# Kernel optimization log

Hardware: AMD Instinct MI355X
Metric: run time of the kernel (lower is better)

## Reference

```python
import jax, jax.numpy as jnp
import numpy as np

H = 1024          # hidden_size
D = 4             # num_domains
B, S = 8, 2048


def setup_inputs() -> dict:
    key = jax.random.key(0)
    ks = jax.random.split(key, 12)
    inp = {
        "sequence_embeddings": jax.random.normal(ks[0], (B, S, H), jnp.float32),
        "volatility": jax.random.uniform(ks[1], (B, S, 1), jnp.float32) * 0.02 + 0.005,
        "risk_factors": jax.random.normal(ks[2], (B, S, 1), jnp.float32) * 0.01,
        # learned parameters (match torch init scales)
        "domain_feature_weights": jax.random.normal(ks[3], (H, 2 * H), jnp.float32) * 0.02,
        "domain_feature_bias": jnp.zeros((2 * H,), jnp.float32),
        "domain_classifier_weights": jax.random.normal(ks[4], (2 * H, D), jnp.float32) * 0.02,
        "domain_classifier_bias": jnp.zeros((D,), jnp.float32),
        "volatility_router_weights": jax.random.normal(ks[5], (1, 8, D), jnp.float32) * 0.1,
        "volatility_router_bias": jnp.zeros((8, D), jnp.float32),
        "risk_router_weights": jax.random.normal(ks[6], (1, 8, D), jnp.float32) * 0.1,
        "risk_router_bias": jnp.zeros((8, D), jnp.float32),
        "stats_router_weights": jax.random.normal(ks[7], (3, 12, D), jnp.float32) * 0.1,
        "stats_router_bias": jnp.zeros((12, D), jnp.float32),
        "expert_weights": jax.random.normal(ks[8], (D, 2 * H, H), jnp.float32) * 0.02,
        "expert_bias": jnp.zeros((D, H), jnp.float32),
    }
    return inp


def reference(sequence_embeddings, volatility, risk_factors,
              domain_feature_weights, domain_feature_bias,
              domain_classifier_weights, domain_classifier_bias,
              volatility_router_weights, volatility_router_bias,
              risk_router_weights, risk_router_bias,
              stats_router_weights, stats_router_bias,
              expert_weights, expert_bias):
    x = sequence_embeddings
    # shared domain feature extractor: [B,S,H] -> [B,S,2H]
    feat = jnp.tanh(jnp.einsum('bsh,hf->bsf', x, domain_feature_weights) + domain_feature_bias)
    # content-based domain logits [B,S,D]
    dom_logits = jnp.einsum('bsf,fd->bsd', feat, domain_classifier_weights) + domain_classifier_bias
    # volatility router: scalar -> 8 hidden units per domain, tanh, sum -> [B,S,D]
    vol_logits = jnp.tanh(volatility[..., None] * volatility_router_weights[0]
                          + volatility_router_bias).sum(axis=-2)
    # risk router, same structure
    risk_logits = jnp.tanh(risk_factors[..., None] * risk_router_weights[0]
                           + risk_router_bias).sum(axis=-2)
    # per-token statistics (mean/std/max over feature dim) -> [B,S,3]
    stats = jnp.stack([x.mean(axis=-1), x.std(axis=-1), x.max(axis=-1)], axis=-1)
    stats_logits = jnp.tanh(jnp.einsum('bsc,ckd->bskd', stats, stats_router_weights)
                            + stats_router_bias).sum(axis=-2)
    # combined routing distribution over domains
    routing_probs = jax.nn.softmax(dom_logits + vol_logits + risk_logits + stats_logits, axis=-1)
    # dispatch every token through all D experts: [B,S,D,H]
    expert_out = jnp.einsum('bsf,dfh->bsdh', feat, expert_weights) + expert_bias
    # gated combine: [B,S,H]
    out = jnp.einsum('bsd,bsdh->bsh', routing_probs, expert_out)
    return out
```

## Files before the change

### kernel.cpp

```cpp
#include <hip/hip_runtime.h>
#include <hip/hip_bf16.h>
#include <cstdint>
#include <cstddef>

typedef __bf16 bf16_t;
typedef bf16_t bf16x8 __attribute__((ext_vector_type(8)));
typedef bf16_t bf16x4 __attribute__((ext_vector_type(4)));
typedef float  f32x4  __attribute__((ext_vector_type(4)));

#define TOK 16384
#define Hh  1024
#define F2  2048
#define NC  4096

__device__ __forceinline__ void gload_lds16(const bf16_t* g, bf16_t* lds) {
  __builtin_amdgcn_global_load_lds(
      (const __attribute__((address_space(1))) void*)g,
      (__attribute__((address_space(3))) void*)lds, 16, 0, 0);
}

__global__ __launch_bounds__(256)
void k_tr_wf(const float* __restrict__ in, bf16_t* __restrict__ out) {
  __shared__ float T[64][65];
  const int f0 = blockIdx.x * 64, h0 = blockIdx.y * 64;
  const int tid = threadIdx.x;
  const int c4 = (tid & 15) * 4, r = tid >> 4;
  #pragma unroll
  for (int p = 0; p < 4; ++p) {
    int hh = p * 16 + r;
    float4 v = *(const float4*)&in[(size_t)(h0 + hh) * F2 + f0 + c4];
    T[c4 + 0][hh] = v.x; T[c4 + 1][hh] = v.y; T[c4 + 2][hh] = v.z; T[c4 + 3][hh] = v.w;
  }
  __syncthreads();
  #pragma unroll
  for (int p = 0; p < 4; ++p) {
    int ff = p * 16 + r;
    bf16x4 o = { (bf16_t)T[ff][c4 + 0], (bf16_t)T[ff][c4 + 1],
                 (bf16_t)T[ff][c4 + 2], (bf16_t)T[ff][c4 + 3] };
    *(bf16x4*)&out[(size_t)(f0 + ff) * Hh + h0 + c4] = o;
  }
}

__global__ __launch_bounds__(256)
void k_tr_we(const float* __restrict__ in, bf16_t* __restrict__ out) {
  __shared__ float T[64][65];
  const int f0 = blockIdx.x * 64, h0 = blockIdx.y * 64, d = blockIdx.z;
  const float* ind = in + (size_t)d * F2 * Hh;
  const int tid = threadIdx.x;
  const int c4 = (tid & 15) * 4, r = tid >> 4;
  #pragma unroll
  for (int p = 0; p < 4; ++p) {
    int ff = p * 16 + r;
    float4 v = *(const float4*)&ind[(size_t)(f0 + ff) * Hh + h0 + c4];
    T[c4 + 0][ff] = v.x; T[c4 + 1][ff] = v.y; T[c4 + 2][ff] = v.z; T[c4 + 3][ff] = v.w;
  }
  __syncthreads();
  #pragma unroll
  for (int p = 0; p < 4; ++p) {
    int hh = p * 16 + r;
    bf16x4 o = { (bf16_t)T[hh][c4 + 0], (bf16_t)T[hh][c4 + 1],
                 (bf16_t)T[hh][c4 + 2], (bf16_t)T[hh][c4 + 3] };
    *(bf16x4*)&out[(size_t)((h0 + hh) * 4 + d) * F2 + f0 + c4] = o;
  }
}

__global__ void k_router_w(const float* __restrict__ x, const float* __restrict__ vol,
                           const float* __restrict__ risk, const float* __restrict__ clsb,
                           const float* __restrict__ vw, const float* __restrict__ vb,
                           const float* __restrict__ rw, const float* __restrict__ rb,
                           const float* __restrict__ sw, const float* __restrict__ sb,
                           bf16_t* __restrict__ xbf, float* __restrict__ LP,
                           int m0, int Tc) {
  int w = threadIdx.x >> 6, l = threadIdx.x & 63;
  int t = blockIdx.x * 4 + w;
  if (t >= Tc) return;
  int s = m0 + t;
  const float4* xr = (const float4*)(x + (size_t)s * Hh);
  bf16x4* xo = (bf16x4*)(xbf + (size_t)s * Hh);
  float sum = 0.f, sq = 0.f, mx = -1e30f;
  #pragma unroll
  for (int it = 0; it < 4; ++it) {
    float4 v = xr[it * 64 + l];
    sum += v.x + v.y + v.z + v.w;
    sq  += v.x * v.x + v.y * v.y + v.z * v.z + v.w * v.w;
    mx = fmaxf(mx, fmaxf(fmaxf(v.x, v.y), fmaxf(v.z, v.w)));
    bf16x4 o = { (bf16_t)v.x, (bf16_t)v.y, (bf16_t)v.z, (bf16_t)v.w };
    xo[it * 64 + l] = o;
  }
  #pragma unroll
  for (int off = 32; off; off >>= 1) {
    sum += __shfl_xor(sum, off, 64);
    sq  += __shfl_xor(sq,  off, 64);
    mx   = fmaxf(mx, __shfl_xor(mx, off, 64));
  }
  if (l < 4) {
    int d = l;
    float mean = sum * (1.0f / Hh);
    float var  = sq * (1.0f / Hh) - mean * mean;
    float sd   = sqrtf(fmaxf(var, 0.f));
    float v = vol[s], rk = risk[s];
    float acc = clsb[d];
    #pragma unroll
    for (int k = 0; k < 8; ++k)  acc += tanhf(v  * vw[k*4+d] + vb[k*4+d]);
    #pragma unroll
    for (int k = 0; k < 8; ++k)  acc += tanhf(rk * rw[k*4+d] + rb[k*4+d]);
    #pragma unroll
    for (int k = 0; k < 12; ++k)
      acc += tanhf(mean * sw[k*4+d] + sd * sw[48 + k*4+d] + mx * sw[96 + k*4+d] + sb[k*4+d]);
    LP[t * 4 + d] = acc;
  }
}

__global__ void k_dom(const bf16_t* __restrict__ feat, const float* __restrict__ Wc,
                      float* __restrict__ LP) {
  int w = threadIdx.x >> 6, l = threadIdx.x & 63;
  int t = blockIdx.x * 4 + w;
  const bf16_t* fr = feat + (size_t)t * F2;
  const float4* Wc4 = (const float4*)Wc;
  float a0 = 0, a1 = 0, a2 = 0, a3 = 0;
  #pragma unroll
  for (int it = 0; it < 4; ++it) {
    int f0 = it * 512 + l * 8;
    bf16x8 v = *(const bf16x8*)(fr + f0);
    #pragma unroll
    for (int j = 0; j < 8; ++j) {
      float vf = (float)v[j];
      float4 wv = Wc4[f0 + j];
      a0 += vf * wv.x; a1 += vf * wv.y; a2 += vf * wv.z; a3 += vf * wv.w;
    }
  }
  #pragma unroll
  for (int off = 32; off; off >>= 1) {
    a0 += __shfl_xor(a0, off, 64); a1 += __shfl_xor(a1, off, 64);
    a2 += __shfl_xor(a2, off, 64); a3 += __shfl_xor(a3, off, 64);
  }
  if (l == 0) {
    float l0 = a0 + LP[t*4+0], l1 = a1 + LP[t*4+1];
    float l2 = a2 + LP[t*4+2], l3 = a3 + LP[t*4+3];
    float m = fmaxf(fmaxf(l0, l1), fmaxf(l2, l3));
    float e0 = expf(l0 - m), e1 = expf(l1 - m), e2 = expf(l2 - m), e3 = expf(l3 - m);
    float inv = 1.f / (e0 + e1 + e2 + e3);
    LP[t*4+0] = e0 * inv; LP[t*4+1] = e1 * inv; LP[t*4+2] = e2 * inv; LP[t*4+3] = e3 * inv;
  }
}

__global__ __launch_bounds__(512, 1)
void k_feat_gemm256(const bf16_t* __restrict__ A, const bf16_t* __restrict__ Bt,
                    const float* __restrict__ bias, bf16_t* __restrict__ feat, int nbm) {
  constexpr int K = Hh, NT = K / 32;
  __shared__ bf16_t lds[4 * 8192 * 2];
  bf16_t* ldsB = lds + 32768;
  const int tid = threadIdx.x;
  const int l = tid & 63, wid = tid >> 6;
  const int wm = wid >> 2, wn = wid & 3;
  const int l15 = l & 15, lg = l >> 4;

  const int nwg = nbm * 8, cpx = nwg >> 3;
  int swzb = (blockIdx.x & 7) * cpx + (blockIdx.x >> 3);
  const int bm = swzb % nbm, bn = swzb / nbm;

  const bf16_t* gA = A  + (size_t)(bm * 256) * K;
  const bf16_t* gB = Bt + (size_t)(bn * 256) * K;

  int s_row[2], s_gx[2];
  #pragma unroll
  for (int i = 0; i < 2; ++i) {
    int slot = i * 512 + tid;
    s_row[i] = slot >> 2;
    s_gx[i]  = ((slot & 3) ^ ((s_row[i] >> 1) & 3)) << 3;
  }

  #define GLOAD(g, ts) do {                                                   \
    if ((g) < 2)                                                              \
      gload_lds16(gA + (size_t)s_row[g] * K + (ts) * 32 + s_gx[g],            \
                  lds  + ((ts) & 3) * 8192 + ((g) * 512 + tid) * 8);          \
    else                                                                      \
      gload_lds16(gB + (size_t)s_row[(g)-2] * K + (ts) * 32 + s_gx[(g)-2],    \
                  ldsB + ((ts) & 3) * 8192 + (((g)-2) * 512 + tid) * 8);      \
  } while (0)
  #define FENCE asm volatile("" ::: "memory")
  #define SB0 __builtin_amdgcn_sched_barrier(0)

  const int cswz = ((lg ^ ((l15 >> 1) & 3)) << 3);
  f32x4 acc[8][4] = {};
  bf16x8 bE[4], aE[4], bO[4], aO[4], aH[4];

  #pragma unroll
  for (int g = 0; g < 4; ++g) GLOAD(g, 0);
  #pragma unroll
  for (int g = 0; g < 4; ++g) GLOAD(g, 1);
  #pragma unroll
  for (int g = 0; g < 4; ++g) GLOAD(g, 2);
  asm volatile("s_waitcnt vmcnt(4)" ::: "memory");
  FENCE; __builtin_amdgcn_s_barrier(); FENCE;
  #pragma unroll
  for (int ni = 0; ni < 4; ++ni)
    bE[ni] = *(const bf16x8*)&ldsB[(wn * 64 + ni * 16 + l15) * 32 + cswz];
  #pragma unroll
  for (int mi = 0; mi < 4; ++mi)
    aE[mi] = *(const bf16x8*)&lds[(wm * 128 + mi * 16 + l15) * 32 + cswz];

  #define MFMA8(q, f0, f1, bset)                                               \
    __builtin_amdgcn_s_setprio(1);                                             \
    _Pragma("unroll")                                                          \
    for (int ni = 0; ni < 4; ++ni) {                                           \
      acc[q][ni]   = __builtin_amdgcn_mfma_f32_16x16x32_bf16(f0, bset[ni], acc[q][ni],   0, 0, 0); \
      acc[q+1][ni] = __builtin_amdgcn_mfma_f32_16x16x32_bf16(f1, bset[ni], acc[q+1][ni], 0, 0, 0); \
    }                                                                          \
    __builtin_amdgcn_s_setprio(0)

  #define TILE(T, bC, aC, bN, aN, DOSTAGE, DOREADS, VMODE)                     \
  {                                                                            \
    const bf16_t* AsC = lds  + ((T) & 3) * 8192;                               \
    const bf16_t* AsN = lds  + (((T) + 1) & 3) * 8192;                         \
    const bf16_t* BsN = ldsB + (((T) + 1) & 3) * 8192;                         \
    if (DOSTAGE) GLOAD(0, (T) + 3);                                            \
    _Pragma("unroll")                                                          \
    for (int mi = 0; mi < 4; ++mi)                                             \
      aH[mi] = *(const bf16x8*)&AsC[(wm * 128 + 64 + mi * 16 + l15) * 32 + cswz]; \
    SB0;                                                                       \
    MFMA8(0, aC[0], aC[1], bC);                                                \
    SB0;                                                                       \
    if (DOSTAGE) GLOAD(1, (T) + 3);                                            \
    if (DOREADS) {                                                             \
      _Pragma("unroll")                                                        \
      for (int ni = 0; ni < 4; ++ni)                                           \
        bN[ni] = *(const bf16x8*)&BsN[(wn * 64 + ni * 16 + l15) * 32 + cswz];  \
    }                                                                          \
    SB0;                                                                       \
    MFMA8(2, aC[2], aC[3], bC);                                                \
    SB0;                                                                       \
    if (DOSTAGE) GLOAD(2, (T) + 3);                                            \
    if (DOREADS) {                                                             \
      _Pragma("unroll")                                                        \
      for (int mi = 0; mi < 4; ++mi)                                           \
        aN[mi] = *(const bf16x8*)&AsN[(wm * 128 + mi * 16 + l15) * 32 + cswz]; \
    }                                                                          \
    SB0;                                                                       \
    MFMA8(4, aH[0], aH[1], bC);                                                \
    SB0;                                                                       \
    if (VMODE == 1)      asm volatile("s_waitcnt vmcnt(3)" ::: "memory");      \
    else if (VMODE == 2) asm volatile("s_waitcnt vmcnt(0)" ::: "memory");      \
    if (DOSTAGE) GLOAD(3, (T) + 3);                                            \
    SB0;                                                                       \
    MFMA8(6, aH[2], aH[3], bC);                                                \
    FENCE; __builtin_amdgcn_s_barrier(); FENCE;                                \
  }

  for (int tp = 0; tp < NT - 4; tp += 2) {
    TILE(tp,     bE, aE, bO, aO, true, true, 1);
    TILE(tp + 1, bO, aO, bE, aE, true, true, 1);
  }
  TILE(NT - 4, bE, aE, bO, aO, true,  true,  1);
  TILE(NT - 3, bO, aO, bE, aE, false, true,  2);
  TILE(NT - 2, bE, aE, bO, aO, false, true,  0);
  TILE(NT - 1, bO, aO, bE, aE, false, false, 0);
  #undef TILE
  #undef MFMA8
  #undef GLOAD
  #undef FENCE
  #undef SB0

  #pragma unroll
  for (int ni = 0; ni < 4; ++ni) {
    int gn = bn * 256 + wn * 64 + ni * 16 + l15;
    float bv = bias[gn];
    #pragma unroll
    for (int mi = 0; mi < 8; ++mi) {
      int gmBase = bm * 256 + wm * 128 + mi * 16 + lg * 4;
      #pragma unroll
      for (int r = 0; r < 4; ++r)
        feat[(size_t)(gmBase + r) * F2 + gn] = (bf16_t)tanhf(acc[mi][ni][r] + bv);
    }
  }
}

__global__ __launch_bounds__(512, 1)
void k_expert_gemm256(const bf16_t* __restrict__ A, const bf16_t* __restrict__ Bt,
                      const float* __restrict__ P, const float* __restrict__ EB,
                      float* __restrict__ out, int nbm) {
  constexpr int K = F2, NT = K / 32;
  __shared__ bf16_t lds[4 * 8192 * 2];
  bf16_t* ldsB = lds + 32768;
  const int tid = threadIdx.x;
  const int l = tid & 63, wid = tid >> 6;
  const int wm = wid >> 2, wn = wid & 3;
  const int l15 = l & 15, lg = l >> 4;

  const int nwg = nbm * 16, cpx = nwg >> 3;
  int swzb = (blockIdx.x & 7) * cpx + (blockIdx.x >> 3);
  const int bm = swzb % nbm, bn = swzb / nbm;

  const bf16_t* gA = A  + (size_t)(bm * 256) * K;
  const bf16_t* gB = Bt + (size_t)(bn * 256) * K;

  int s_row[2], s_gx[2];
  #pragma unroll
  for (int i = 0; i < 2; ++i) {
    int slot = i * 512 + tid;
    s_row[i] = slot >> 2;
    s_gx[i]  = ((slot & 3) ^ ((s_row[i] >> 1) & 3)) << 3;
  }

  #define GLOAD(g, ts) do {                                                   \
    if ((g) < 2)                                                              \
      gload_lds16(gA + (size_t)s_row[g] * K + (ts) * 32 + s_gx[g],            \
                  lds  + ((ts) & 3) * 8192 + ((g) * 512 + tid) * 8);          \
    else                                                                      \
      gload_lds16(gB + (size_t)s_row[(g)-2] * K + (ts) * 32 + s_gx[(g)-2],    \
                  ldsB + ((ts) & 3) * 8192 + (((g)-2) * 512 + tid) * 8);      \
  } while (0)
  #define FENCE asm volatile("" ::: "memory")
  #define SB0 __builtin_amdgcn_sched_barrier(0)

  const int cswz = ((lg ^ ((l15 >> 1) & 3)) << 3);
  f32x4 acc[8][4] = {};
  bf16x8 bE[4], aE[4], bO[4], aO[4], aH[4];

  #pragma unroll
  for (int g = 0; g < 4; ++g) GLOAD(g, 0);
  #pragma unroll
  for (int g = 0; g < 4; ++g) GLOAD(g, 1);
  #pragma unroll
  for (int g = 0; g < 4; ++g) GLOAD(g, 2);
  asm volatile("s_waitcnt vmcnt(4)" ::: "memory");
  FENCE; __builtin_amdgcn_s_barrier(); FENCE;
  #pragma unroll
  for (int ni = 0; ni < 4; ++ni)
    bE[ni] = *(const bf16x8*)&ldsB[(wn * 64 + ni * 16 + l15) * 32 + cswz];
  #pragma unroll
  for (int mi = 0; mi < 4; ++mi)
    aE[mi] = *(const bf16x8*)&lds[(wm * 128 + mi * 16 + l15) * 32 + cswz];

  #define MFMA8(q, f0, f1, bset)                                               \
    __builtin_amdgcn_s_setprio(1);                                             \
    _Pragma("unroll")                                                          \
    for (int ni = 0; ni < 4; ++ni) {                                           \
      acc[q][ni]   = __builtin_amdgcn_mfma_f32_16x16x32_bf16(f0, bset[ni], acc[q][ni],   0, 0, 0); \
      acc[q+1][ni] = __builtin_amdgcn_mfma_f32_16x16x32_bf16(f1, bset[ni], acc[q+1][ni], 0, 0, 0); \
    }                                                                          \
    __builtin_amdgcn_s_setprio(0)

  #define TILE(T, bC, aC, bN, aN, DOSTAGE, DOREADS, VMODE)                     \
  {                                                                            \
    const bf16_t* AsC = lds  + ((T) & 3) * 8192;                               \
    const bf16_t* AsN = lds  + (((T) + 1) & 3) * 8192;                         \
    const bf16_t* BsN = ldsB + (((T) + 1) & 3) * 8192;                         \
    if (DOSTAGE) GLOAD(0, (T) + 3);                                            \
    _Pragma("unroll")                                                          \
    for (int mi = 0; mi < 4; ++mi)                                             \
      aH[mi] = *(const bf16x8*)&AsC[(wm * 128 + 64 + mi * 16 + l15) * 32 + cswz]; \
    SB0;                                                                       \
    MFMA8(0, aC[0], aC[1], bC);                                                \
    SB0;                                                                       \
    if (DOSTAGE) GLOAD(1, (T) + 3);                                            \
    if (DOREADS) {                                                             \
      _Pragma("unroll")                                                        \
      for (int ni = 0; ni < 4; ++ni)                                           \
        bN[ni] = *(const bf16x8*)&BsN[(wn * 64 + ni * 16 + l15) * 32 + cswz];  \
    }                                                                          \
    SB0;                                                                       \
    MFMA8(2, aC[2], aC[3], bC);                                                \
    SB0;                                                                       \
    if (DOSTAGE) GLOAD(2, (T) + 3);                                            \
    if (DOREADS) {                                                             \
      _Pragma("unroll")                                                        \
      for (int mi = 0; mi < 4; ++mi)                                           \
        aN[mi] = *(const bf16x8*)&AsN[(wm * 128 + mi * 16 + l15) * 32 + cswz]; \
    }                                                                          \
    SB0;                                                                       \
    MFMA8(4, aH[0], aH[1], bC);                                                \
    SB0;                                                                       \
    if (VMODE == 1)      asm volatile("s_waitcnt vmcnt(3)" ::: "memory");      \
    else if (VMODE == 2) asm volatile("s_waitcnt vmcnt(0)" ::: "memory");      \
    if (DOSTAGE) GLOAD(3, (T) + 3);                                            \
    SB0;                                                                       \
    MFMA8(6, aH[2], aH[3], bC);                                                \
    FENCE; __builtin_amdgcn_s_barrier(); FENCE;                                \
  }

  for (int tp = 0; tp < NT - 4; tp += 2) {
    TILE(tp,     bE, aE, bO, aO, true, true, 1);
    TILE(tp + 1, bO, aO, bE, aE, true, true, 1);
  }
  TILE(NT - 4, bE, aE, bO, aO, true,  true,  1);
  TILE(NT - 3, bO, aO, bE, aE, false, true,  2);
  TILE(NT - 2, bE, aE, bO, aO, false, true,  0);
  TILE(NT - 1, bO, aO, bE, aE, false, false, 0);
  #undef TILE
  #undef MFMA8
  #undef GLOAD
  #undef FENCE
  #undef SB0

  #pragma unroll
  for (int mi = 0; mi < 8; ++mi) {
    int gmBase = bm * 256 + wm * 128 + mi * 16 + lg * 4;
    float pr[4];
    #pragma unroll
    for (int r = 0; r < 4; ++r) pr[r] = P[(gmBase + r) * 4 + (l & 3)];
    #pragma unroll
    for (int ni = 0; ni < 4; ++ni) {
      int colp = bn * 256 + wn * 64 + ni * 16 + l15;
      int h = colp >> 2;
      #pragma unroll
      for (int r = 0; r < 4; ++r) {
        float sv = acc[mi][ni][r] * pr[r];
        sv += __shfl_xor(sv, 1, 64);
        sv += __shfl_xor(sv, 2, 64);
        if ((l & 3) == 0) {
          int gm = gmBase + r;
          float bt = P[gm*4+0]*EB[h] + P[gm*4+1]*EB[Hh+h]
                   + P[gm*4+2]*EB[2*Hh+h] + P[gm*4+3]*EB[3*Hh+h];
          out[(size_t)gm * Hh + h] = sv + bt;
        }
      }
    }
  }
}

extern "C" void kernel_launch(void* const* d_in, const int* in_sizes, int n_in,
                              void* d_out, int out_size, void* d_ws, size_t ws_size,
                              hipStream_t stream) {
  const float *x  = (const float*)d_in[0],  *vol = (const float*)d_in[1];
  const float *risk = (const float*)d_in[2], *Wf = (const float*)d_in[3];
  const float *fb = (const float*)d_in[4],  *Wc = (const float*)d_in[5];
  const float *cb = (const float*)d_in[6],  *vw = (const float*)d_in[7];
  const float *vb = (const float*)d_in[8],  *rw = (const float*)d_in[9];
  const float *rb = (const float*)d_in[10], *sw = (const float*)d_in[11];
  const float *sb = (const float*)d_in[12], *We = (const float*)d_in[13];
  const float *eb = (const float*)d_in[14];

  float* out = (float*)d_out;
  char* ws = (char*)d_ws;
  const size_t KB = 1024, MB = 1024 * 1024;

  float*  LP  = (float*) ws;
  bf16_t* wft = (bf16_t*)(ws + 256 * KB);
  bf16_t* wet = (bf16_t*)(ws + 256 * KB + 4 * MB);
  bf16_t* xbf = (bf16_t*)(ws + 256 * KB + 20 * MB);
  const size_t base = 256 * KB + 52 * MB;
  int Tc = TOK;
  while (Tc > 1024 && base + (size_t)Tc * F2 * sizeof(bf16_t) > ws_size) Tc >>= 1;
  bf16_t* feat = (bf16_t*)(ws + base);

  k_tr_wf <<<dim3(F2 / 64, Hh / 64), 256, 0, stream>>>(Wf, wft);
  k_tr_we <<<dim3(F2 / 64, Hh / 64, 4), 256, 0, stream>>>(We, wet);

  for (int m0 = 0; m0 < TOK; m0 += Tc) {
    k_router_w<<<Tc / 4, 256, 0, stream>>>(
        x, vol, risk, cb, vw, vb, rw, rb, sw, sb, xbf, LP, m0, Tc);
    int nbmF = Tc / 256;
    k_feat_gemm256<<<nbmF * (F2 / 256), 512, 0, stream>>>(
        xbf + (size_t)m0 * Hh, wft, fb, feat, nbmF);
    k_dom<<<Tc / 4, 256, 0, stream>>>(feat, Wc, LP);
    k_expert_gemm256<<<nbmF * (NC / 256), 512, 0, stream>>>(
        feat, wet, LP, eb, out + (size_t)m0 * Hh, nbmF);
  }
}
```

Before: 545.9 us.

## Quantize expert GEMM to int8 with per-column weight scales and int8 features

Switches the expert GEMM from bf16 MFMA to int8 MFMA (16x16x64), storing tanh features as int8 scaled by 127 and expert weights as int8 with per-output-column absmax scales computed by two new kernels. The dequantization is folded into the routing-weighted epilogue, and the domain classifier reads the int8 features. This targets the dominant expert GEMM cost by doubling MFMA throughput and halving operand bandwidth. The price is lower precision: 8-bit features and weights add quantization error that may exceed tolerance. The per-column scale pass also reads all expert weights again on every call.

New measurement: 487.9 us. 1.12x faster.

```diff
diff --git a/kernel.cpp b/kernel.cpp
--- a/kernel.cpp
+++ b/kernel.cpp
@@ -7,6 +7,7 @@
 typedef bf16_t bf16x8 __attribute__((ext_vector_type(8)));
 typedef bf16_t bf16x4 __attribute__((ext_vector_type(4)));
 typedef float  f32x4  __attribute__((ext_vector_type(4)));
+typedef int    i32x4  __attribute__((ext_vector_type(4)));
 
 #define TOK 16384
 #define Hh  1024
@@ -14,6 +15,11 @@
 #define NC  4096
 
 __device__ __forceinline__ void gload_lds16(const bf16_t* g, bf16_t* lds) {
+  __builtin_amdgcn_global_load_lds(
+      (const __attribute__((address_space(1))) void*)g,
+      (__attribute__((address_space(3))) void*)lds, 16, 0, 0);
+}
+__device__ __forceinline__ void gload_lds16b(const int8_t* g, int8_t* lds) {
   __builtin_amdgcn_global_load_lds(
       (const __attribute__((address_space(1))) void*)g,
       (__attribute__((address_space(3))) void*)lds, 16, 0, 0);
@@ -41,8 +47,27 @@
   }
 }
 
+__global__ void k_we_scale1(const float* __restrict__ We, float* __restrict__ pmax) {
+  int ht = blockIdx.x, fc = blockIdx.y, d = blockIdx.z;
+  int h = ht * 256 + threadIdx.x;
+  float m = 0.f;
+  for (int ff = 0; ff < 256; ++ff) {
+    float v = We[((size_t)d * F2 + fc * 256 + ff) * Hh + h];
+    m = fmaxf(m, fabsf(v));
+  }
+  pmax[(size_t)(h * 4 + d) * 8 + fc] = m;
+}
+__global__ void k_we_scale2(const float* __restrict__ pmax, float* __restrict__ SB) {
+  int cp = blockIdx.x * 256 + threadIdx.x;
+  float m = 0.f;
+  #pragma unroll
+  for (int i = 0; i < 8; ++i) m = fmaxf(m, pmax[(size_t)cp * 8 + i]);
+  SB[cp] = m;
+}
+
 __global__ __launch_bounds__(256)
-void k_tr_we(const float* __restrict__ in, bf16_t* __restrict__ out) {
+void k_tr_we(const float* __restrict__ in, const float* __restrict__ SB,
+             int8_t* __restrict__ out) {
   __shared__ float T[64][65];
   const int f0 = blockIdx.x * 64, h0 = blockIdx.y * 64, d = blockIdx.z;
   const float* ind = in + (size_t)d * F2 * Hh;
@@ -58,9 +83,15 @@
   #pragma unroll
   for (int p = 0; p < 4; ++p) {
     int hh = p * 16 + r;
-    bf16x4 o = { (bf16_t)T[hh][c4 + 0], (bf16_t)T[hh][c4 + 1],
-                 (bf16_t)T[hh][c4 + 2], (bf16_t)T[hh][c4 + 3] };
-    *(bf16x4*)&out[(size_t)((h0 + hh) * 4 + d) * F2 + f0 + c4] = o;
+    int cp = (h0 + hh) * 4 + d;
+    float m = SB[cp];
+    float inv = (m > 1e-30f) ? 127.f / m : 0.f;
+    char4 o;
+    o.x = (int8_t)__float2int_rn(T[hh][c4 + 0] * inv);
+    o.y = (int8_t)__float2int_rn(T[hh][c4 + 1] * inv);
+    o.z = (int8_t)__float2int_rn(T[hh][c4 + 2] * inv);
+    o.w = (int8_t)__float2int_rn(T[hh][c4 + 3] * inv);
+    *(char4*)&out[(size_t)cp * F2 + f0 + c4] = o;
   }
 }
 
@@ -111,20 +142,21 @@
   }
 }
 
-__global__ void k_dom(const bf16_t* __restrict__ feat, const float* __restrict__ Wc,
+__global__ void k_dom(const int8_t* __restrict__ feat, const float* __restrict__ Wc,
                       float* __restrict__ LP) {
   int w = threadIdx.x >> 6, l = threadIdx.x & 63;
   int t = blockIdx.x * 4 + w;
-  const bf16_t* fr = feat + (size_t)t * F2;
+  const int8_t* fr = feat + (size_t)t * F2;
   const float4* Wc4 = (const float4*)Wc;
   float a0 = 0, a1 = 0, a2 = 0, a3 = 0;
   #pragma unroll
   for (int it = 0; it < 4; ++it) {
     int f0 = it * 512 + l * 8;
-    bf16x8 v = *(const bf16x8*)(fr + f0);
+    int2 v = *(const int2*)(fr + f0);
     #pragma unroll
     for (int j = 0; j < 8; ++j) {
-      float vf = (float)v[j];
+      int word = (j < 4) ? v.x : v.y;
+      float vf = (float)((signed char)(word >> (8 * (j & 3)))) * (1.f / 127.f);
       float4 wv = Wc4[f0 + j];
       a0 += vf * wv.x; a1 += vf * wv.y; a2 += vf * wv.z; a3 += vf * wv.w;
     }
@@ -146,7 +178,7 @@
 
 __global__ __launch_bounds__(512, 1)
 void k_feat_gemm256(const bf16_t* __restrict__ A, const bf16_t* __restrict__ Bt,
-                    const float* __restrict__ bias, bf16_t* __restrict__ feat, int nbm) {
+                    const float* __restrict__ bias, int8_t* __restrict__ feat, int nbm) {
   constexpr int K = Hh, NT = K / 32;
   __shared__ bf16_t lds[4 * 8192 * 2];
   bf16_t* ldsB = lds + 32768;
@@ -269,19 +301,21 @@
     for (int mi = 0; mi < 8; ++mi) {
       int gmBase = bm * 256 + wm * 128 + mi * 16 + lg * 4;
       #pragma unroll
-      for (int r = 0; r < 4; ++r)
-        feat[(size_t)(gmBase + r) * F2 + gn] = (bf16_t)tanhf(acc[mi][ni][r] + bv);
+      for (int r = 0; r < 4; ++r) {
+        float t = tanhf(acc[mi][ni][r] + bv);
+        feat[(size_t)(gmBase + r) * F2 + gn] = (int8_t)__float2int_rn(t * 127.f);
+      }
     }
   }
 }
 
 __global__ __launch_bounds__(512, 1)
-void k_expert_gemm256(const bf16_t* __restrict__ A, const bf16_t* __restrict__ Bt,
+void k_expert_gemm256(const int8_t* __restrict__ A, const int8_t* __restrict__ Bt,
                       const float* __restrict__ P, const float* __restrict__ EB,
-                      float* __restrict__ out, int nbm) {
-  constexpr int K = F2, NT = K / 32;
-  __shared__ bf16_t lds[4 * 8192 * 2];
-  bf16_t* ldsB = lds + 32768;
+                      const float* __restrict__ SBq, float* __restrict__ out, int nbm) {
+  constexpr int K = F2, NT = K / 64;
+  __shared__ int8_t lds[4 * 16384 * 2];
+  int8_t* ldsB = lds + 65536;
   const int tid = threadIdx.x;
   const int l = tid & 63, wid = tid >> 6;
   const int wm = wid >> 2, wn = wid & 3;
@@ -291,31 +325,31 @@
   int swzb = (blockIdx.x & 7) * cpx + (blockIdx.x >> 3);
   const int bm = swzb % nbm, bn = swzb / nbm;
 
-  const bf16_t* gA = A  + (size_t)(bm * 256) * K;
-  const bf16_t* gB = Bt + (size_t)(bn * 256) * K;
-
-  int s_row[2], s_gx[2];
+  const int8_t* gA = A  + (size_t)(bm * 256) * K;
+  const int8_t* gB = Bt + (size_t)(bn * 256) * K;
+
+  int s_row[2], s_gxB[2];
   #pragma unroll
   for (int i = 0; i < 2; ++i) {
     int slot = i * 512 + tid;
-    s_row[i] = slot >> 2;
-    s_gx[i]  = ((slot & 3) ^ ((s_row[i] >> 1) & 3)) << 3;
+    s_row[i]  = slot >> 2;
+    s_gxB[i]  = ((slot & 3) ^ ((s_row[i] >> 1) & 3)) << 4;
   }
 
   #define GLOAD(g, ts) do {                                                   \
     if ((g) < 2)                                                              \
-      gload_lds16(gA + (size_t)s_row[g] * K + (ts) * 32 + s_gx[g],            \
-                  lds  + ((ts) & 3) * 8192 + ((g) * 512 + tid) * 8);          \
+      gload_lds16b(gA + (size_t)s_row[g] * K + (ts) * 64 + s_gxB[g],          \
+                   lds  + ((ts) & 3) * 16384 + ((g) * 512 + tid) * 16);       \
     else                                                                      \
-      gload_lds16(gB + (size_t)s_row[(g)-2] * K + (ts) * 32 + s_gx[(g)-2],    \
-                  ldsB + ((ts) & 3) * 8192 + (((g)-2) * 512 + tid) * 8);      \
+      gload_lds16b(gB + (size_t)s_row[(g)-2] * K + (ts) * 64 + s_gxB[(g)-2],  \
+                   ldsB + ((ts) & 3) * 16384 + (((g)-2) * 512 + tid) * 16);   \
   } while (0)
   #define FENCE asm volatile("" ::: "memory")
   #define SB0 __builtin_amdgcn_sched_barrier(0)
 
-  const int cswz = ((lg ^ ((l15 >> 1) & 3)) << 3);
-  f32x4 acc[8][4] = {};
-  bf16x8 bE[4], aE[4], bO[4], aO[4], aH[4];
+  const int cswzB = ((lg ^ ((l15 >> 1) & 3)) << 4);
+  i32x4 acc[8][4] = {};
+  i32x4 bE[4], aE[4], bO[4], aO[4], aH[4];
 
   #pragma unroll
   for (int g = 0; g < 4; ++g) GLOAD(g, 0);
@@ -327,29 +361,29 @@
   FENCE; __builtin_amdgcn_s_barrier(); FENCE;
   #pragma unroll
   for (int ni = 0; ni < 4; ++ni)
-    bE[ni] = *(const bf16x8*)&ldsB[(wn * 64 + ni * 16 + l15) * 32 + cswz];
+    bE[ni] = *(const i32x4*)&ldsB[(wn * 64 + ni * 16 + l15) * 64 + cswzB];
   #pragma unroll
   for (int mi = 0; mi < 4; ++mi)
-    aE[mi] = *(const bf16x8*)&lds[(wm * 128 + mi * 16 + l15) * 32 + cswz];
+    aE[mi] = *(const i32x4*)&lds[(wm * 128 + mi * 16 + l15) * 64 + cswzB];
 
   #define MFMA8(q, f0, f1, bset)                                               \
     __builtin_amdgcn_s_setprio(1);                                             \
     _Pragma("unroll")                                                          \
     for (int ni = 0; ni < 4; ++ni) {                                           \
-      acc[q][ni]   = __builtin_amdgcn_mfma_f32_16x16x32_bf16(f0, bset[ni], acc[q][ni],   0, 0, 0); \
-      acc[q+1][ni] = __builtin_amdgcn_mfma_f32_16x16x32_bf16(f1, bset[ni], acc[q+1][ni], 0, 0, 0); \
+      acc[q][ni]   = __builtin_amdgcn_mfma_i32_16x16x64_i8(f0, bset[ni], acc[q][ni],   0, 0, 0); \
+      acc[q+1][ni] = __builtin_amdgcn_mfma_i32_16x16x64_i8(f1, bset[ni], acc[q+1][ni], 0, 0, 0); \
     }                                                                          \
     __builtin_amdgcn_s_setprio(0)
 
   #define TILE(T, bC, aC, bN, aN, DOSTAGE, DOREADS, VMODE)                     \
   {                                                                            \
-    const bf16_t* AsC = lds  + ((T) & 3) * 8192;                               \
-    const bf16_t* AsN = lds  + (((T) + 1) & 3) * 8192;                         \
-    const bf16_t* BsN = ldsB + (((T) + 1) & 3) * 8192;                         \
+    const int8_t* AsC = lds  + ((T) & 3) * 16384;                              \
+    const int8_t* AsN = lds  + (((T) + 1) & 3) * 16384;                        \
+    const int8_t* BsN = ldsB + (((T) + 1) & 3) * 16384;                        \
     if (DOSTAGE) GLOAD(0, (T) + 3);                                            \
     _Pragma("unroll")                                                          \
     for (int mi = 0; mi < 4; ++mi)                                             \
-      aH[mi] = *(const bf16x8*)&AsC[(wm * 128 + 64 + mi * 16 + l15) * 32 + cswz]; \
+      aH[mi] = *(const i32x4*)&AsC[(wm * 128 + 64 + mi * 16 + l15) * 64 + cswzB]; \
     SB0;                                                                       \
     MFMA8(0, aC[0], aC[1], bC);                                                \
     SB0;                                                                       \
@@ -357,7 +391,7 @@
     if (DOREADS) {                                                             \
       _Pragma("unroll")                                                        \
       for (int ni = 0; ni < 4; ++ni)                                           \
-        bN[ni] = *(const bf16x8*)&BsN[(wn * 64 + ni * 16 + l15) * 32 + cswz];  \
+        bN[ni] = *(const i32x4*)&BsN[(wn * 64 + ni * 16 + l15) * 64 + cswzB];  \
     }                                                                          \
     SB0;                                                                       \
     MFMA8(2, aC[2], aC[3], bC);                                                \
@@ -366,7 +400,7 @@
     if (DOREADS) {                                                             \
       _Pragma("unroll")                                                        \
       for (int mi = 0; mi < 4; ++mi)                                           \
-        aN[mi] = *(const bf16x8*)&AsN[(wm * 128 + mi * 16 + l15) * 32 + cswz]; \
+        aN[mi] = *(const i32x4*)&AsN[(wm * 128 + mi * 16 + l15) * 64 + cswzB]; \
     }                                                                          \
     SB0;                                                                       \
     MFMA8(4, aH[0], aH[1], bC);                                                \
@@ -403,9 +437,10 @@
     for (int ni = 0; ni < 4; ++ni) {
       int colp = bn * 256 + wn * 64 + ni * 16 + l15;
       int h = colp >> 2;
+      float dq = SBq[colp] * (1.0f / 16129.0f);
       #pragma unroll
       for (int r = 0; r < 4; ++r) {
-        float sv = acc[mi][ni][r] * pr[r];
+        float sv = (float)acc[mi][ni][r] * dq * pr[r];
         sv += __shfl_xor(sv, 1, 64);
         sv += __shfl_xor(sv, 2, 64);
         if ((l & 3) == 0) {
@@ -435,17 +470,21 @@
   char* ws = (char*)d_ws;
   const size_t KB = 1024, MB = 1024 * 1024;
 
-  float*  LP  = (float*) ws;
-  bf16_t* wft = (bf16_t*)(ws + 256 * KB);
-  bf16_t* wet = (bf16_t*)(ws + 256 * KB + 4 * MB);
-  bf16_t* xbf = (bf16_t*)(ws + 256 * KB + 20 * MB);
-  const size_t base = 256 * KB + 52 * MB;
+  float*  LP     = (float*) ws;
+  float*  SBq    = (float*) (ws + 256 * KB);
+  float*  pmax   = (float*) (ws + 512 * KB);
+  bf16_t* wft    = (bf16_t*)(ws + 1 * MB);
+  int8_t* wet    = (int8_t*)(ws + 5 * MB);
+  bf16_t* xbf    = (bf16_t*)(ws + 13 * MB);
+  const size_t base = 45 * MB;
   int Tc = TOK;
-  while (Tc > 1024 && base + (size_t)Tc * F2 * sizeof(bf16_t) > ws_size) Tc >>= 1;
-  bf16_t* feat = (bf16_t*)(ws + base);
-
-  k_tr_wf <<<dim3(F2 / 64, Hh / 64), 256, 0, stream>>>(Wf, wft);
-  k_tr_we <<<dim3(F2 / 64, Hh / 64, 4), 256, 0, stream>>>(We, wet);
+  while (Tc > 1024 && base + (size_t)Tc * F2 > ws_size) Tc >>= 1;
+  int8_t* feat = (int8_t*)(ws + base);
+
+  k_tr_wf    <<<dim3(F2 / 64, Hh / 64), 256, 0, stream>>>(Wf, wft);
+  k_we_scale1<<<dim3(4, 8, 4), 256, 0, stream>>>(We, pmax);
+  k_we_scale2<<<16, 256, 0, stream>>>(pmax, SBq);
+  k_tr_we    <<<dim3(F2 / 64, Hh / 64, 4), 256, 0, stream>>>(We, SBq, wet);
 
   for (int m0 = 0; m0 < TOK; m0 += Tc) {
     k_router_w<<<Tc / 4, 256, 0, stream>>>(
@@ -455,6 +494,6 @@
         xbf + (size_t)m0 * Hh, wft, fb, feat, nbmF);
     k_dom<<<Tc / 4, 256, 0, stream>>>(feat, Wc, LP);
     k_expert_gemm256<<<nbmF * (NC / 256), 512, 0, stream>>>(
-        feat, wet, LP, eb, out + (size_t)m0 * Hh, nbmF);
-  }
-}
+        feat, wet, LP, eb, SBq, out + (size_t)m0 * Hh, nbmF);
+  }
+}
```
